# Kernel optimization log

Hardware: AMD Instinct MI355X
Metric: run time of the kernel (lower is better)

Reference implementation:

```python
import jax, jax.numpy as jnp
import numpy as np

T, IN, M, C, OUT = 8192, 1024, 64, 16, 1024  # time, input, trace, context, output


def _ln(x, eps=1e-5):
    mu = jnp.mean(x, axis=-1, keepdims=True)
    var = jnp.var(x, axis=-1, keepdims=True)
    return (x - mu) * jax.lax.rsqrt(var + eps)


def _mish(x):
    return x * jnp.tanh(jax.nn.softplus(x))


def setup_inputs() -> dict:
    key = jax.random.key(0)
    ks = jax.random.split(key, 8)

    def w(k, o, i):
        return (jax.random.normal(k, (o, i), jnp.float32) / np.sqrt(i).astype(np.float32))

    return {
        "x": jax.random.normal(ks[0], (T, IN), jnp.float32),
        "state0": jnp.zeros((1, M, C), jnp.float32),  # real part of complex zero init
        "start": jax.random.uniform(ks[1], (T,)) < 0.002,  # sparse episode resets
        "next_done": jnp.zeros((T,), bool),  # unused by the sequential-equivalent math
        "a": jnp.linspace(1e-6, 0.5, M, dtype=jnp.float32),  # ffa.init decay
        "bf": (2.0 * jnp.pi / jnp.linspace(1.0, 1024.0, C)).astype(jnp.float32),  # ffa.init freqs
        "pre_w": w(ks[2], M, IN), "pre_b": jnp.zeros((M,), jnp.float32),
        "skip_w": w(ks[3], OUT, IN), "skip_b": jnp.zeros((OUT,), jnp.float32),
        "mix_w1": w(ks[4], M * C, 2 * M * C), "mix_b1": jnp.zeros((M * C,), jnp.float32),
        "mix_w2": w(ks[5], M * C, M * C), "mix_b2": jnp.zeros((M * C,), jnp.float32),
        "mix_w3": w(ks[6], OUT, M * C), "mix_b3": jnp.zeros((OUT,), jnp.float32),
    }


def _forward(x, state0, start, a, bf, pre_w, pre_b, skip_w, skip_b,
             mix_w1, mix_b1, mix_w2, mix_b2, mix_w3, mix_b3):
    Tn = x.shape[0]
    # pre = softplus(Linear(LayerNorm(x)))  -> [T, M]
    pre = jax.nn.softplus(_ln(x) @ pre_w.T + pre_b)
    # one-step FFA decay gamma[m,c] = exp(-|a_m| + i*b_c)
    la = jnp.broadcast_to(-jnp.abs(a)[:, None], (a.shape[0], bf.shape[0]))
    lb = jnp.broadcast_to(bf[None, :], la.shape)
    gamma = jnp.exp(jax.lax.complex(la, lb))  # [M, C] complex64
    # reset monoid: s_t = A_t * s_{t-1} + b_t,  A_t = 0 where episode starts
    A = jnp.where(start[:, None, None], jnp.zeros((), gamma.dtype), gamma[None])  # [T,M,C]
    b_el = jnp.broadcast_to(pre[:, :, None].astype(gamma.dtype), A.shape)  # [T,M,C]
    s_init = state0.astype(gamma.dtype)  # [1, M, C]
    b_el = b_el.at[0].add(A[0] * s_init[0])  # fold carried state into first element

    def combine(lhs, rhs):
        Al, bl = lhs
        Ar, br = rhs
        return Ar * Al, Ar * bl + br

    _, s = jax.lax.associative_scan(combine, (A, b_el))  # s: [T, M, C] states at every t

    s_flat = s.reshape(Tn, M * C)
    # global (all-element) complex mean / real std normalization, as in the source
    scaled = (s_flat - jnp.mean(s_flat)) / (1e-6 + jnp.std(s_flat))
    z = jnp.concatenate([scaled.real, scaled.imag], axis=-1)  # [T, 2*M*C]
    z = _mish(z @ mix_w1.T + mix_b1)
    z = _mish(z @ mix_w2.T + mix_b2)
    z = z @ mix_w3.T + mix_b3  # [T, OUT]
    out = _ln(z + (x @ skip_w.T + skip_b))
    return out, s[-1:]


def reference(x, state0, start, next_done, a, bf, pre_w, pre_b, skip_w, skip_b,
              mix_w1, mix_b1, mix_w2, mix_b2, mix_w3, mix_b3):
    return _forward(x, state0, start, a, bf, pre_w, pre_b, skip_w, skip_b,
                    mix_w1, mix_b1, mix_w2, mix_b2, mix_w3, mix_b3)
```

## Files before the change

### kernel.cpp

```cpp
#include <hip/hip_runtime.h>
#include <hip/hip_bf16.h>

#define T_    8192
#define INDIM 1024
#define MTR   64
#define CCTX  16
#define MC    1024
#define NOUT  1024
#define CHUNK 64
#define NCH   128

using bf16x8 = __attribute__((ext_vector_type(8))) short;
using f32x4  = __attribute__((ext_vector_type(4))) float;

__device__ __forceinline__ unsigned short f2bf(float f) {
  unsigned int u = __builtin_bit_cast(unsigned int, f);
  u += 0x7fffu + ((u >> 16) & 1u);
  return (unsigned short)(u >> 16);
}
__device__ __forceinline__ float bf2f(unsigned short u) {
  return __builtin_bit_cast(float, (unsigned int)u << 16);
}

__device__ __forceinline__ float mish_f(float v) {
  float u = __expf(v);
  float w = u * (u + 2.f);
  return (v > 20.f) ? v : v * __fdividef(w, w + 2.f);
}

typedef __attribute__((address_space(1))) void gas_void;
typedef __attribute__((address_space(3))) void las_void;

__device__ __forceinline__ void gload_lds16(const void* g, void* l) {
  __builtin_amdgcn_global_load_lds((gas_void*)g, (las_void*)l, 16, 0, 0);
}

__global__ __launch_bounds__(256) void cast4_k(const float* __restrict__ w1, const float* __restrict__ w2,
                                               const float* __restrict__ w3, const float* __restrict__ sw,
                                               unsigned short* __restrict__ o1, unsigned short* __restrict__ o2,
                                               unsigned short* __restrict__ o3, unsigned short* __restrict__ o4) {
  long i = ((long)blockIdx.x * 256 + threadIdx.x) * 4;
  const float* src; unsigned short* dst; long off;
  if (i < 2097152)      { src = w1; dst = o1; off = i; }
  else if (i < 3145728) { src = w2; dst = o2; off = i - 2097152; }
  else if (i < 4194304) { src = w3; dst = o3; off = i - 3145728; }
  else if (i < 5242880) { src = sw; dst = o4; off = i - 4194304; }
  else return;
  float4 v = *(const float4*)(src + off);
  ushort4 o = { f2bf(v.x), f2bf(v.y), f2bf(v.z), f2bf(v.w) };
  *(ushort4*)(dst + off) = o;
}

__device__ __forceinline__ float2 block_sum2(float s, float ss, float* sbuf) {
#pragma unroll
  for (int off = 32; off > 0; off >>= 1) {
    s  += __shfl_down(s, off);
    ss += __shfl_down(ss, off);
  }
  if ((threadIdx.x & 63) == 0) {
    sbuf[(threadIdx.x >> 6) * 2]     = s;
    sbuf[(threadIdx.x >> 6) * 2 + 1] = ss;
  }
  __syncthreads();
  return make_float2(sbuf[0] + sbuf[2] + sbuf[4] + sbuf[6],
                     sbuf[1] + sbuf[3] + sbuf[5] + sbuf[7]);
}

__global__ __launch_bounds__(256) void wsum_k(const float* __restrict__ w1,
                                              float* __restrict__ wre, float* __restrict__ wim) {
  __shared__ float sbuf[8];
  const long row = blockIdx.x;
  const float4* r4 = (const float4*)(w1 + row * 2048);
  float4 a = r4[threadIdx.x];
  float4 b = r4[256 + threadIdx.x];
  float2 t = block_sum2(a.x + a.y + a.z + a.w, b.x + b.y + b.z + b.w, sbuf);
  if (threadIdx.x == 0) { wre[row] = t.x; wim[row] = t.y; }
}

__global__ __launch_bounds__(256) void ln_cast_k(const float* __restrict__ x,
                                                 float2* __restrict__ rowstat,
                                                 unsigned short* __restrict__ xb) {
  __shared__ float sbuf[8];
  const long row = blockIdx.x;
  float4 v = ((const float4*)(x + (row << 10)))[threadIdx.x];
  ushort4 c = { f2bf(v.x), f2bf(v.y), f2bf(v.z), f2bf(v.w) };
  ((ushort4*)(xb + (row << 10)))[threadIdx.x] = c;
  float2 t = block_sum2(v.x + v.y + v.z + v.w,
                        v.x * v.x + v.y * v.y + v.z * v.z + v.w * v.w, sbuf);
  float mean = t.x * (1.f / 1024.f);
  float var  = t.y * (1.f / 1024.f) - mean * mean;
  float rstd = rsqrtf(var + 1e-5f);
  if (threadIdx.x == 0) rowstat[row] = make_float2(mean, rstd);
}

__global__ __launch_bounds__(256) void ln_out1b_k(const unsigned short* __restrict__ p, float* __restrict__ out) {
  __shared__ float sbuf[8];
  const long row = blockIdx.x;
  ushort4 u4 = ((const ushort4*)(p + (row << 10)))[threadIdx.x];
  float4 v = { bf2f(u4.x), bf2f(u4.y), bf2f(u4.z), bf2f(u4.w) };
  float2 t = block_sum2(v.x + v.y + v.z + v.w,
                        v.x * v.x + v.y * v.y + v.z * v.z + v.w * v.w, sbuf);
  float mean = t.x * (1.f / 1024.f);
  float var  = t.y * (1.f / 1024.f) - mean * mean;
  float rstd = rsqrtf(var + 1e-5f);
  float4 o = { (v.x - mean) * rstd, (v.y - mean) * rstd,
               (v.z - mean) * rstd, (v.w - mean) * rstd };
  ((float4*)(out + (row << 10)))[threadIdx.x] = o;
}

__global__ __launch_bounds__(256) void pre_part_k(const float* __restrict__ x,
                                                  const float2* __restrict__ rowstat,
                                                  const float* __restrict__ pw,
                                                  float* __restrict__ part) {
  const int lane = threadIdx.x & 63;
  const int wvu  = __builtin_amdgcn_readfirstlane(threadIdx.x >> 6);
  const int kc   = blockIdx.y;
  const int r0   = (blockIdx.x * 4 + wvu) * 32;

  const float* wrow = pw + (long)lane * 1024 + kc * 128;
  float wreg[128];
#pragma unroll
  for (int j = 0; j < 32; ++j)
    *(float4*)&wreg[j * 4] = ((const float4*)wrow)[j];
  float swsum = 0.f;
#pragma unroll
  for (int j = 0; j < 128; ++j) swsum += wreg[j];

  float* po = part + ((long)kc * T_ + r0) * 64 + lane;
  const float* xbase = x + (long)r0 * 1024 + kc * 128;

  for (int i = 0; i < 32; i += 2) {
    const float4* xr0 = (const float4*)(xbase + (long)i * 1024);
    const float4* xr1 = (const float4*)(xbase + (long)(i + 1) * 1024);
    float a0 = 0.f, a1 = 0.f, a2 = 0.f, a3 = 0.f;
    float b0 = 0.f, b1 = 0.f, b2 = 0.f, b3 = 0.f;
#pragma unroll
    for (int j = 0; j < 32; j += 4) {
      float4 xa0 = xr0[j],     xa1 = xr0[j + 1], xa2 = xr0[j + 2], xa3 = xr0[j + 3];
      float4 xb0 = xr1[j],     xb1 = xr1[j + 1], xb2 = xr1[j + 2], xb3 = xr1[j + 3];
      a0 += wreg[4*j+0]*xa0.x  + wreg[4*j+1]*xa0.y  + wreg[4*j+2]*xa0.z  + wreg[4*j+3]*xa0.w;
      a1 += wreg[4*j+4]*xa1.x  + wreg[4*j+5]*xa1.y  + wreg[4*j+6]*xa1.z  + wreg[4*j+7]*xa1.w;
      a2 += wreg[4*j+8]*xa2.x  + wreg[4*j+9]*xa2.y  + wreg[4*j+10]*xa2.z + wreg[4*j+11]*xa2.w;
      a3 += wreg[4*j+12]*xa3.x + wreg[4*j+13]*xa3.y + wreg[4*j+14]*xa3.z + wreg[4*j+15]*xa3.w;
      b0 += wreg[4*j+0]*xb0.x  + wreg[4*j+1]*xb0.y  + wreg[4*j+2]*xb0.z  + wreg[4*j+3]*xb0.w;
      b1 += wreg[4*j+4]*xb1.x  + wreg[4*j+5]*xb1.y  + wreg[4*j+6]*xb1.z  + wreg[4*j+7]*xb1.w;
      b2 += wreg[4*j+8]*xb2.x  + wreg[4*j+9]*xb2.y  + wreg[4*j+10]*xb2.z + wreg[4*j+11]*xb2.w;
      b3 += wreg[4*j+12]*xb3.x + wreg[4*j+13]*xb3.y + wreg[4*j+14]*xb3.z + wreg[4*j+15]*xb3.w;
    }
    float2 s0 = rowstat[r0 + i];
    float2 s1 = rowstat[r0 + i + 1];
    po[(long)i * 64]       = s0.y * ((a0 + a1) + (a2 + a3)) - s0.x * s0.y * swsum;
    po[(long)(i + 1) * 64] = s1.y * ((b0 + b1) + (b2 + b3)) - s1.x * s1.y * swsum;
  }
}

__global__ __launch_bounds__(256) void pre_fin_k(const float* __restrict__ part,
                                                 const float* __restrict__ pb,
                                                 float* __restrict__ pre) {
  long i = (long)blockIdx.x * 256 + threadIdx.x;
  int m = (int)(i & 63);
  float s = 0.f;
#pragma unroll
  for (int kc = 0; kc < 8; ++kc)
    s += part[(long)kc * T_ * 64 + i];
  float v = s + pb[m];
  float sp = fmaxf(v, 0.f) + log1pf(expf(-fabsf(v)));
  pre[i] = sp;
}

__global__ __launch_bounds__(256) void scan_p1(const float* __restrict__ pre, const int* __restrict__ start,
                                               const float* __restrict__ a, const float* __restrict__ bfr,
                                               double2* __restrict__ chA, double2* __restrict__ chB) {
  int ch = blockIdx.y * 256 + threadIdx.x;
  int m = ch >> 4, c = ch & 15;
  double dec = exp(-fabs((double)a[m]));
  double th = (double)bfr[c];
  double gre = dec * cos(th), gim = dec * sin(th);
  int j = blockIdx.x;
  int t0 = j * CHUNK;
  double pr = 1.0, pi = 0.0, sr = 0.0, si = 0.0;
  for (int t = t0; t < t0 + CHUNK; ++t) {
    double b = (double)pre[(long)t * 64 + m];
    if (start[t]) {
      pr = 0.0; pi = 0.0; sr = b; si = 0.0;
    } else {
      double nsr = gre * sr - gim * si + b;
      si = gre * si + gim * sr; sr = nsr;
      double npr = gre * pr - gim * pi;
      pi = gre * pi + gim * pr; pr = npr;
    }
  }
  chA[j * MC + ch] = make_double2(pr, pi);
  chB[j * MC + ch] = make_double2(sr, si);
}

__global__ __launch_bounds__(64) void scan_p2(const double2* __restrict__ chA, const double2* __restrict__ chB,
                                              const float* __restrict__ state0,
                                              double2* __restrict__ carry, double* __restrict__ red,
                                              float* __restrict__ out_tail, int fmt) {
  if (blockIdx.x == 0 && threadIdx.x < 4) red[threadIdx.x] = 0.0;
  int ch = blockIdx.x * 64 + threadIdx.x;
  double cr = (double)state0[ch], ci = 0.0;
  for (int j = 0; j < NCH; ++j) {
    carry[j * MC + ch] = make_double2(cr, ci);
    double2 A = chA[j * MC + ch];
    double2 B = chB[j * MC + ch];
    double ncr = A.x * cr - A.y * ci + B.x;
    ci = A.x * ci + A.y * cr + B.y;
    cr = ncr;
  }
  if (fmt == 1024) {
    out_tail[ch] = (float)cr;
  } else {
    out_tail[2 * ch]     = (float)cr;
    out_tail[2 * ch + 1] = (float)ci;
  }
}

__global__ __launch_bounds__(256) void scan_p3(const float* __restrict__ pre, const int* __restrict__ start,
                                               const float* __restrict__ a, const float* __restrict__ bfr,
                                               const double2* __restrict__ carry,
                                               double* __restrict__ red,
                                               unsigned short* __restrict__ z) {
  __shared__ double sbuf[12];
  int ch = blockIdx.y * 256 + threadIdx.x;
  int m = ch >> 4, c = ch & 15;
  double dec = exp(-fabs((double)a[m]));
  double th = (double)bfr[c];
  double gre = dec * cos(th), gim = dec * sin(th);
  int j = blockIdx.x;
  int t0 = j * CHUNK;
  double2 cin = carry[j * MC + ch];
  double sr = cin.x, si = cin.y;
  double aR = 0.0, aI = 0.0, aS = 0.0;
  for (int t = t0; t < t0 + CHUNK; ++t) {
    double b = (double)pre[(long)t * 64 + m];
    if (start[t]) { sr = b; si = 0.0; }
    else {
      double nsr = gre * sr - gim * si + b;
      si = gre * si + gim * sr; sr = nsr;
    }
    z[(long)t * 2048 + ch]        = f2bf((float)sr);
    z[(long)t * 2048 + 1024 + ch] = f2bf((float)si);
    aR += sr; aI += si; aS += sr * sr + si * si;
  }
#pragma unroll
  for (int off = 32; off > 0; off >>= 1) {
    aR += __shfl_down(aR, off); aI += __shfl_down(aI, off); aS += __shfl_down(aS, off);
  }
  if ((threadIdx.x & 63) == 0) {
    int w = threadIdx.x >> 6;
    sbuf[w * 3] = aR; sbuf[w * 3 + 1] = aI; sbuf[w * 3 + 2] = aS;
  }
  __syncthreads();
  if (threadIdx.x == 0) {
    atomicAdd(&red[0], sbuf[0] + sbuf[3] + sbuf[6] + sbuf[9]);
    atomicAdd(&red[1], sbuf[1] + sbuf[4] + sbuf[7] + sbuf[10]);
    atomicAdd(&red[2], sbuf[2] + sbuf[5] + sbuf[8] + sbuf[11]);
  }
}

__global__ void finalize_red(const double* __restrict__ red, float* __restrict__ redf) {
  const double n = (double)T_ * (double)MC;
  double mre = red[0] / n, mim = red[1] / n;
  double var = red[2] / n - mre * mre - mim * mim;
  double sd = sqrt(var > 0.0 ? var : 0.0);
  redf[0] = (float)mre;
  redf[1] = (float)mim;
  redf[2] = (float)(1.0 / (1e-6 + sd));
}

#define TSZ (128 * 32)
template<int EP>
__device__ __forceinline__ void gemm128_core(const unsigned short* __restrict__ A,
                                             const unsigned short* __restrict__ B,
                                             const float* __restrict__ bias,
                                             const unsigned short* __restrict__ addb,
                                             const float* __restrict__ redf,
                                             const float* __restrict__ wre,
                                             const float* __restrict__ wim,
                                             void* __restrict__ Cout,
                                             int bx, int by, int N_, int K_,
                                             unsigned short* lA, unsigned short* lB) {
  const int tid = threadIdx.x;
  const int lane = tid & 63;
  const int wv = tid >> 6;
  const int wr = wv >> 1, wc = wv & 1;
  const long brow = (long)bx * 128;
  const long bcol = (long)by * 128;

  f32x4 acc[4][4];
#pragma unroll
  for (int i = 0; i < 4; i++)
#pragma unroll
    for (int j = 0; j < 4; j++)
      acc[i][j] = f32x4{0.f, 0.f, 0.f, 0.f};

  const int c0 = tid, c1 = tid + 256;
  const long ar0 = brow + (c0 >> 2), ar1 = brow + (c1 >> 2);
  const long br0 = bcol + (c0 >> 2), br1 = bcol + (c1 >> 2);
  const int ko0 = (((c0 & 3) ^ ((c0 >> 3) & 3)) * 8);
  const int ko1 = (((c1 & 3) ^ ((c1 >> 3) & 3)) * 8);
  const int r15 = lane & 15;
  const int swzq = (((lane >> 4) ^ ((r15 >> 1) & 3)) * 8);

  const int nt = K_ >> 5;

#define STAGE(ti, bu)                                                      \
  do {                                                                     \
    gload_lds16(A + ar0 * K_ + (ti) * 32 + ko0, lA + (bu) * TSZ + c0 * 8); \
    gload_lds16(A + ar1 * K_ + (ti) * 32 + ko1, lA + (bu) * TSZ + c1 * 8); \
    gload_lds16(B + br0 * K_ + (ti) * 32 + ko0, lB + (bu) * TSZ + c0 * 8); \
    gload_lds16(B + br1 * K_ + (ti) * 32 + ko1, lB + (bu) * TSZ + c1 * 8); \
  } while (0)

  STAGE(0, 0);
  STAGE(1, 1);

  for (int i = 0; i < nt; ++i) {
    if (i + 2 < nt) {
      STAGE(i + 2, (i + 2) & 3);
      asm volatile("s_waitcnt vmcnt(8)" ::: "memory");
    } else if (i + 1 < nt) {
      asm volatile("s_waitcnt vmcnt(4)" ::: "memory");
    } else {
      asm volatile("s_waitcnt vmcnt(0)" ::: "memory");
    }
    __builtin_amdgcn_sched_barrier(0);
    __builtin_amdgcn_s_barrier();
    __builtin_amdgcn_sched_barrier(0);

    const unsigned short* bA = lA + (i & 3) * TSZ;
    const unsigned short* bB = lB + (i & 3) * TSZ;
    bf16x8 af[4], bv[4];
#pragma unroll
    for (int mi = 0; mi < 4; mi++)
      af[mi] = *(const bf16x8*)&bA[(wr * 64 + mi * 16 + r15) * 32 + swzq];
#pragma unroll
    for (int nj = 0; nj < 4; nj++)
      bv[nj] = *(const bf16x8*)&bB[(wc * 64 + nj * 16 + r15) * 32 + swzq];
#pragma unroll
    for (int mi = 0; mi < 4; mi++)
#pragma unroll
      for (int nj = 0; nj < 4; nj++)
        acc[mi][nj] = __builtin_amdgcn_mfma_f32_16x16x32_bf16(af[mi], bv[nj], acc[mi][nj], 0, 0, 0);
  }
#undef STAGE

  float cre = 0.f, cim = 0.f, inv = 1.f;
  if (EP == 4) { cre = redf[0]; cim = redf[1]; inv = redf[2]; }

  const int rq = (lane >> 4) * 4;
#pragma unroll
  for (int nj = 0; nj < 4; nj++) {
    const long col = bcol + wc * 64 + nj * 16 + r15;
    const float bs = bias[col];
    float wrc = 0.f, wic = 0.f;
    if (EP == 4) { wrc = wre[col]; wic = wim[col]; }
#pragma unroll
    for (int mi = 0; mi < 4; mi++) {
#pragma unroll
      for (int r = 0; r < 4; r++) {
        const long row = brow + wr * 64 + mi * 16 + rq + r;
        float va = acc[mi][nj][r];
        if (EP == 1) {
          ((unsigned short*)Cout)[row * N_ + col] = f2bf(va + bs);
        } else if (EP == 3) {
          float v = va + bs + bf2f(addb[row * N_ + col]);
          ((unsigned short*)Cout)[row * N_ + col] = f2bf(v);
        } else if (EP == 4) {
          float v = (va - cre * wrc - cim * wic) * inv + bs;
          ((unsigned short*)Cout)[row * N_ + col] = f2bf(mish_f(v));
        } else {
          ((unsigned short*)Cout)[row * N_ + col] = f2bf(mish_f(va + bs));
        }
      }
    }
  }
}

template<int EP>
__global__ __launch_bounds__(256) void gemm128_k(const unsigned short* __restrict__ A,
                                                 const unsigned short* __restrict__ B,
                                                 const float* __restrict__ bias,
                                                 const unsigned short* __restrict__ addb,
                                                 void* __restrict__ Cout, int N_, int K_) {
  __shared__ __align__(16) unsigned short lA[4 * TSZ];
  __shared__ __align__(16) unsigned short lB[4 * TSZ];
  gemm128_core<EP>(A, B, bias, addb, nullptr, nullptr, nullptr, Cout,
                   blockIdx.x, blockIdx.y, N_, K_, lA, lB);
}

__global__ __launch_bounds__(256) void gemm_dual128(const unsigned short* __restrict__ A1,
                                                    const unsigned short* __restrict__ B1,
                                                    const float* __restrict__ bias1,
                                                    unsigned short* __restrict__ C1, int K1,
                                                    const float* __restrict__ redf,
                                                    const float* __restrict__ wre,
                                                    const float* __restrict__ wim,
                                                    const unsigned short* __restrict__ A2,
                                                    const unsigned short* __restrict__ B2,
                                                    const float* __restrict__ bias2,
                                                    unsigned short* __restrict__ C2, int K2) {
  __shared__ __align__(16) unsigned short lA[4 * TSZ];
  __shared__ __align__(16) unsigned short lB[4 * TSZ];
  int b = blockIdx.x;
  if (b < 512) {
    gemm128_core<4>(A1, B1, bias1, nullptr, redf, wre, wim, C1, b & 63, b >> 6, 1024, K1, lA, lB);
  } else {
    b -= 512;
    gemm128_core<1>(A2, B2, bias2, nullptr, nullptr, nullptr, nullptr, C2, b & 63, b >> 6, 1024, K2, lA, lB);
  }
}

extern "C" void kernel_launch(void* const* d_in, const int* in_sizes, int n_in,
                              void* d_out, int out_size, void* d_ws, size_t ws_size,
                              hipStream_t stream) {
  (void)in_sizes; (void)n_in; (void)ws_size;
  const float* x      = (const float*)d_in[0];
  const float* state0 = (const float*)d_in[1];
  const int*   start  = (const int*)d_in[2];
  const float* a      = (const float*)d_in[4];
  const float* bfr    = (const float*)d_in[5];
  const float* pre_w  = (const float*)d_in[6];
  const float* pre_b  = (const float*)d_in[7];
  const float* skip_w = (const float*)d_in[8];
  const float* skip_b = (const float*)d_in[9];
  const float* w1     = (const float*)d_in[10];
  const float* b1     = (const float*)d_in[11];
  const float* w2     = (const float*)d_in[12];
  const float* b2     = (const float*)d_in[13];
  const float* w3     = (const float*)d_in[14];
  const float* b3     = (const float*)d_in[15];

  char* ws = (char*)d_ws;
  const size_t MB = 1u << 20;
  unsigned short* skipb = (unsigned short*)(ws + 0);
  float*          part  = (float*)(ws + 32 * MB);
  unsigned short* h3b   = (unsigned short*)(ws + 48 * MB);
  unsigned short* z     = (unsigned short*)(ws + 64 * MB);
  unsigned short* xb    = (unsigned short*)(ws + 96 * MB);
  unsigned short* h2    = (unsigned short*)(ws + 96 * MB);
  unsigned short* h1    = (unsigned short*)(ws + 112 * MB);
  unsigned short* wb1   = (unsigned short*)(ws + 128 * MB);
  unsigned short* wb2   = (unsigned short*)(ws + 132 * MB);
  unsigned short* wb3   = (unsigned short*)(ws + 134 * MB);
  unsigned short* skwb  = (unsigned short*)(ws + 136 * MB);
  float*          pre   = (float*)(ws + 138 * MB);
  double2*        chA   = (double2*)(ws + 140 * MB);
  double2*        chB   = (double2*)(ws + 142 * MB);
  double2*        carry = (double2*)(ws + 144 * MB);
  double*         red   = (double*)(ws + 146 * MB);
  float*          redf  = (float*)(ws + 146 * MB + 64);
  float2*         rowst = (float2*)(ws + 147 * MB);
  float*          wre   = (float*)(ws + 147 * MB + 65536);
  float*          wim   = (float*)(ws + 147 * MB + 65536 + 4096);

  cast4_k<<<5120, 256, 0, stream>>>(w1, w2, w3, skip_w, wb1, wb2, wb3, skwb);
  wsum_k<<<1024, 256, 0, stream>>>(w1, wre, wim);

  ln_cast_k<<<8192, 256, 0, stream>>>(x, rowst, xb);
  pre_part_k<<<dim3(64, 8), 256, 0, stream>>>(x, rowst, pre_w, part);
  pre_fin_k<<<2048, 256, 0, stream>>>(part, pre_b, pre);

  int tail_elems = out_size - T_ * NOUT;
  float* out_tail = (float*)d_out + (long)T_ * NOUT;
  scan_p1<<<dim3(NCH, 4), 256, 0, stream>>>(pre, start, a, bfr, chA, chB);
  scan_p2<<<16, 64, 0, stream>>>(chA, chB, state0, carry, red, out_tail, tail_elems);
  scan_p3<<<dim3(NCH, 4), 256, 0, stream>>>(pre, start, a, bfr, carry, red, z);
  finalize_red<<<1, 1, 0, stream>>>(red, redf);

  gemm_dual128<<<1024, 256, 0, stream>>>(z, wb1, b1, h1, 2048, redf, wre, wim,
                                         xb, skwb, skip_b, skipb, 1024);
  gemm128_k<2><<<dim3(64, 8), 256, 0, stream>>>(h1, wb2, b2, nullptr, h2, 1024, 1024);
  gemm128_k<3><<<dim3(64, 8), 256, 0, stream>>>(h2, wb3, b3, skipb, h3b, 1024, 1024);

  ln_out1b_k<<<8192, 256, 0, stream>>>(h3b, (float*)d_out);
}
```

Baseline: 277.9 us.

## Merge prep kernels, fuse pre projection, add MFMA priority and XCD-aware block remap

Folds the weight-cast, weight row-sum and LayerNorm-stat kernels into one launch. It replaces the split-K pre projection plus its reduction kernel with a single kernel that loops over all K chunks and applies softplus directly, so the partial-sum buffer goes away. It also raises wave priority around the MFMA block in the GEMM core and remaps block indices so that blocks landing on the same XCD work on neighbouring tiles, aiming for better L2 reuse. These changes cut launch overhead and intermediate traffic, but the pre projection now runs only 256 blocks with a serial K loop, which lowers its parallelism.

```diff
diff --git a/kernel.cpp b/kernel.cpp
--- a/kernel.cpp
+++ b/kernel.cpp
@@ -35,22 +35,6 @@
   __builtin_amdgcn_global_load_lds((gas_void*)g, (las_void*)l, 16, 0, 0);
 }
 
-__global__ __launch_bounds__(256) void cast4_k(const float* __restrict__ w1, const float* __restrict__ w2,
-                                               const float* __restrict__ w3, const float* __restrict__ sw,
-                                               unsigned short* __restrict__ o1, unsigned short* __restrict__ o2,
-                                               unsigned short* __restrict__ o3, unsigned short* __restrict__ o4) {
-  long i = ((long)blockIdx.x * 256 + threadIdx.x) * 4;
-  const float* src; unsigned short* dst; long off;
-  if (i < 2097152)      { src = w1; dst = o1; off = i; }
-  else if (i < 3145728) { src = w2; dst = o2; off = i - 2097152; }
-  else if (i < 4194304) { src = w3; dst = o3; off = i - 3145728; }
-  else if (i < 5242880) { src = sw; dst = o4; off = i - 4194304; }
-  else return;
-  float4 v = *(const float4*)(src + off);
-  ushort4 o = { f2bf(v.x), f2bf(v.y), f2bf(v.z), f2bf(v.w) };
-  *(ushort4*)(dst + off) = o;
-}
-
 __device__ __forceinline__ float2 block_sum2(float s, float ss, float* sbuf) {
 #pragma unroll
   for (int off = 32; off > 0; off >>= 1) {
@@ -66,31 +50,45 @@
                      sbuf[1] + sbuf[3] + sbuf[5] + sbuf[7]);
 }
 
-__global__ __launch_bounds__(256) void wsum_k(const float* __restrict__ w1,
-                                              float* __restrict__ wre, float* __restrict__ wim) {
+__global__ __launch_bounds__(256) void prep_k(const float* __restrict__ w1, const float* __restrict__ w2,
+                                              const float* __restrict__ w3, const float* __restrict__ sw,
+                                              const float* __restrict__ x,
+                                              unsigned short* __restrict__ o1, unsigned short* __restrict__ o2,
+                                              unsigned short* __restrict__ o3, unsigned short* __restrict__ o4,
+                                              float* __restrict__ wre, float* __restrict__ wim,
+                                              float2* __restrict__ rowstat, unsigned short* __restrict__ xb) {
   __shared__ float sbuf[8];
-  const long row = blockIdx.x;
-  const float4* r4 = (const float4*)(w1 + row * 2048);
-  float4 a = r4[threadIdx.x];
-  float4 b = r4[256 + threadIdx.x];
-  float2 t = block_sum2(a.x + a.y + a.z + a.w, b.x + b.y + b.z + b.w, sbuf);
-  if (threadIdx.x == 0) { wre[row] = t.x; wim[row] = t.y; }
-}
-
-__global__ __launch_bounds__(256) void ln_cast_k(const float* __restrict__ x,
-                                                 float2* __restrict__ rowstat,
-                                                 unsigned short* __restrict__ xb) {
-  __shared__ float sbuf[8];
-  const long row = blockIdx.x;
-  float4 v = ((const float4*)(x + (row << 10)))[threadIdx.x];
-  ushort4 c = { f2bf(v.x), f2bf(v.y), f2bf(v.z), f2bf(v.w) };
-  ((ushort4*)(xb + (row << 10)))[threadIdx.x] = c;
-  float2 t = block_sum2(v.x + v.y + v.z + v.w,
-                        v.x * v.x + v.y * v.y + v.z * v.z + v.w * v.w, sbuf);
-  float mean = t.x * (1.f / 1024.f);
-  float var  = t.y * (1.f / 1024.f) - mean * mean;
-  float rstd = rsqrtf(var + 1e-5f);
-  if (threadIdx.x == 0) rowstat[row] = make_float2(mean, rstd);
+  const int b = blockIdx.x;
+  if (b < 5120) {
+    long i = ((long)b * 256 + threadIdx.x) * 4;
+    const float* src; unsigned short* dst; long off;
+    if (i < 2097152)      { src = w1; dst = o1; off = i; }
+    else if (i < 3145728) { src = w2; dst = o2; off = i - 2097152; }
+    else if (i < 4194304) { src = w3; dst = o3; off = i - 3145728; }
+    else if (i < 5242880) { src = sw; dst = o4; off = i - 4194304; }
+    else return;
+    float4 v = *(const float4*)(src + off);
+    ushort4 o = { f2bf(v.x), f2bf(v.y), f2bf(v.z), f2bf(v.w) };
+    *(ushort4*)(dst + off) = o;
+  } else if (b < 6144) {
+    const long row = b - 5120;
+    const float4* r4 = (const float4*)(w1 + row * 2048);
+    float4 a = r4[threadIdx.x];
+    float4 c = r4[256 + threadIdx.x];
+    float2 t = block_sum2(a.x + a.y + a.z + a.w, c.x + c.y + c.z + c.w, sbuf);
+    if (threadIdx.x == 0) { wre[row] = t.x; wim[row] = t.y; }
+  } else {
+    const long row = b - 6144;
+    float4 v = ((const float4*)(x + (row << 10)))[threadIdx.x];
+    ushort4 c = { f2bf(v.x), f2bf(v.y), f2bf(v.z), f2bf(v.w) };
+    ((ushort4*)(xb + (row << 10)))[threadIdx.x] = c;
+    float2 t = block_sum2(v.x + v.y + v.z + v.w,
+                          v.x * v.x + v.y * v.y + v.z * v.z + v.w * v.w, sbuf);
+    float mean = t.x * (1.f / 1024.f);
+    float var  = t.y * (1.f / 1024.f) - mean * mean;
+    float rstd = rsqrtf(var + 1e-5f);
+    if (threadIdx.x == 0) rowstat[row] = make_float2(mean, rstd);
+  }
 }
 
 __global__ __launch_bounds__(256) void ln_out1b_k(const unsigned short* __restrict__ p, float* __restrict__ out) {
@@ -108,64 +106,54 @@
   ((float4*)(out + (row << 10)))[threadIdx.x] = o;
 }
 
-__global__ __launch_bounds__(256) void pre_part_k(const float* __restrict__ x,
-                                                  const float2* __restrict__ rowstat,
-                                                  const float* __restrict__ pw,
-                                                  float* __restrict__ part) {
+__global__ __launch_bounds__(256) void pre_lnproj_k(const float* __restrict__ x,
+                                                    const float2* __restrict__ rowstat,
+                                                    const float* __restrict__ pw,
+                                                    const float* __restrict__ pb,
+                                                    float* __restrict__ pre) {
   const int lane = threadIdx.x & 63;
   const int wvu  = __builtin_amdgcn_readfirstlane(threadIdx.x >> 6);
-  const int kc   = blockIdx.y;
-  const int r0   = (blockIdx.x * 4 + wvu) * 32;
-
-  const float* wrow = pw + (long)lane * 1024 + kc * 128;
-  float wreg[128];
-#pragma unroll
-  for (int j = 0; j < 32; ++j)
-    *(float4*)&wreg[j * 4] = ((const float4*)wrow)[j];
+  const int r0   = blockIdx.x * 32 + wvu * 8;
+
+  float acc[8];
+#pragma unroll
+  for (int r = 0; r < 8; ++r) acc[r] = 0.f;
   float swsum = 0.f;
-#pragma unroll
-  for (int j = 0; j < 128; ++j) swsum += wreg[j];
-
-  float* po = part + ((long)kc * T_ + r0) * 64 + lane;
-  const float* xbase = x + (long)r0 * 1024 + kc * 128;
-
-  for (int i = 0; i < 32; i += 2) {
-    const float4* xr0 = (const float4*)(xbase + (long)i * 1024);
-    const float4* xr1 = (const float4*)(xbase + (long)(i + 1) * 1024);
-    float a0 = 0.f, a1 = 0.f, a2 = 0.f, a3 = 0.f;
-    float b0 = 0.f, b1 = 0.f, b2 = 0.f, b3 = 0.f;
-#pragma unroll
-    for (int j = 0; j < 32; j += 4) {
-      float4 xa0 = xr0[j],     xa1 = xr0[j + 1], xa2 = xr0[j + 2], xa3 = xr0[j + 3];
-      float4 xb0 = xr1[j],     xb1 = xr1[j + 1], xb2 = xr1[j + 2], xb3 = xr1[j + 3];
-      a0 += wreg[4*j+0]*xa0.x  + wreg[4*j+1]*xa0.y  + wreg[4*j+2]*xa0.z  + wreg[4*j+3]*xa0.w;
-      a1 += wreg[4*j+4]*xa1.x  + wreg[4*j+5]*xa1.y  + wreg[4*j+6]*xa1.z  + wreg[4*j+7]*xa1.w;
-      a2 += wreg[4*j+8]*xa2.x  + wreg[4*j+9]*xa2.y  + wreg[4*j+10]*xa2.z + wreg[4*j+11]*xa2.w;
-      a3 += wreg[4*j+12]*xa3.x + wreg[4*j+13]*xa3.y + wreg[4*j+14]*xa3.z + wreg[4*j+15]*xa3.w;
-      b0 += wreg[4*j+0]*xb0.x  + wreg[4*j+1]*xb0.y  + wreg[4*j+2]*xb0.z  + wreg[4*j+3]*xb0.w;
-      b1 += wreg[4*j+4]*xb1.x  + wreg[4*j+5]*xb1.y  + wreg[4*j+6]*xb1.z  + wreg[4*j+7]*xb1.w;
-      b2 += wreg[4*j+8]*xb2.x  + wreg[4*j+9]*xb2.y  + wreg[4*j+10]*xb2.z + wreg[4*j+11]*xb2.w;
-      b3 += wreg[4*j+12]*xb3.x + wreg[4*j+13]*xb3.y + wreg[4*j+14]*xb3.z + wreg[4*j+15]*xb3.w;
+
+  for (int kc = 0; kc < 8; ++kc) {
+    float wreg[128];
+    const float4* wrow4 = (const float4*)(pw + (long)lane * 1024 + kc * 128);
+#pragma unroll
+    for (int j = 0; j < 32; ++j)
+      *(float4*)&wreg[j * 4] = wrow4[j];
+#pragma unroll
+    for (int j = 0; j < 128; ++j) swsum += wreg[j];
+
+    const float* xbase = x + (long)r0 * 1024 + kc * 128;
+#pragma unroll
+    for (int r = 0; r < 8; ++r) {
+      const float4* xr = (const float4*)(xbase + (long)r * 1024);
+      float s0 = 0.f, s1 = 0.f, s2 = 0.f, s3 = 0.f;
+#pragma unroll
+      for (int j = 0; j < 32; j += 4) {
+        float4 x0 = xr[j], x1 = xr[j + 1], x2 = xr[j + 2], x3 = xr[j + 3];
+        s0 += wreg[4*j+0]*x0.x  + wreg[4*j+1]*x0.y  + wreg[4*j+2]*x0.z  + wreg[4*j+3]*x0.w;
+        s1 += wreg[4*j+4]*x1.x  + wreg[4*j+5]*x1.y  + wreg[4*j+6]*x1.z  + wreg[4*j+7]*x1.w;
+        s2 += wreg[4*j+8]*x2.x  + wreg[4*j+9]*x2.y  + wreg[4*j+10]*x2.z + wreg[4*j+11]*x2.w;
+        s3 += wreg[4*j+12]*x3.x + wreg[4*j+13]*x3.y + wreg[4*j+14]*x3.z + wreg[4*j+15]*x3.w;
+      }
+      acc[r] += (s0 + s1) + (s2 + s3);
     }
-    float2 s0 = rowstat[r0 + i];
-    float2 s1 = rowstat[r0 + i + 1];
-    po[(long)i * 64]       = s0.y * ((a0 + a1) + (a2 + a3)) - s0.x * s0.y * swsum;
-    po[(long)(i + 1) * 64] = s1.y * ((b0 + b1) + (b2 + b3)) - s1.x * s1.y * swsum;
-  }
-}
-
-__global__ __launch_bounds__(256) void pre_fin_k(const float* __restrict__ part,
-                                                 const float* __restrict__ pb,
-                                                 float* __restrict__ pre) {
-  long i = (long)blockIdx.x * 256 + threadIdx.x;
-  int m = (int)(i & 63);
-  float s = 0.f;
-#pragma unroll
-  for (int kc = 0; kc < 8; ++kc)
-    s += part[(long)kc * T_ * 64 + i];
-  float v = s + pb[m];
-  float sp = fmaxf(v, 0.f) + log1pf(expf(-fabsf(v)));
-  pre[i] = sp;
+  }
+
+  const float bias = pb[lane];
+#pragma unroll
+  for (int r = 0; r < 8; ++r) {
+    float2 st = rowstat[r0 + r];
+    float v = st.y * acc[r] - st.x * st.y * swsum + bias;
+    float sp = fmaxf(v, 0.f) + log1pf(expf(-fabsf(v)));
+    pre[(long)(r0 + r) * 64 + lane] = sp;
+  }
 }
 
 __global__ __launch_bounds__(256) void scan_p1(const float* __restrict__ pre, const int* __restrict__ start,
@@ -339,11 +327,13 @@
 #pragma unroll
     for (int nj = 0; nj < 4; nj++)
       bv[nj] = *(const bf16x8*)&bB[(wc * 64 + nj * 16 + r15) * 32 + swzq];
+    __builtin_amdgcn_s_setprio(1);
 #pragma unroll
     for (int mi = 0; mi < 4; mi++)
 #pragma unroll
       for (int nj = 0; nj < 4; nj++)
         acc[mi][nj] = __builtin_amdgcn_mfma_f32_16x16x32_bf16(af[mi], bv[nj], acc[mi][nj], 0, 0, 0);
+    __builtin_amdgcn_s_setprio(0);
   }
 #undef STAGE
 
@@ -380,15 +370,16 @@
 }
 
 template<int EP>
-__global__ __launch_bounds__(256) void gemm128_k(const unsigned short* __restrict__ A,
-                                                 const unsigned short* __restrict__ B,
-                                                 const float* __restrict__ bias,
-                                                 const unsigned short* __restrict__ addb,
-                                                 void* __restrict__ Cout, int N_, int K_) {
+__global__ __launch_bounds__(256) void gemm128s_k(const unsigned short* __restrict__ A,
+                                                  const unsigned short* __restrict__ B,
+                                                  const float* __restrict__ bias,
+                                                  const unsigned short* __restrict__ addb,
+                                                  void* __restrict__ Cout, int N_, int K_) {
   __shared__ __align__(16) unsigned short lA[4 * TSZ];
   __shared__ __align__(16) unsigned short lB[4 * TSZ];
+  int comp = (int)((blockIdx.x & 7) * 64 + (blockIdx.x >> 3));
   gemm128_core<EP>(A, B, bias, addb, nullptr, nullptr, nullptr, Cout,
-                   blockIdx.x, blockIdx.y, N_, K_, lA, lB);
+                   comp & 63, comp >> 6, N_, K_, lA, lB);
 }
 
 __global__ __launch_bounds__(256) void gemm_dual128(const unsigned short* __restrict__ A1,
@@ -404,12 +395,12 @@
                                                     unsigned short* __restrict__ C2, int K2) {
   __shared__ __align__(16) unsigned short lA[4 * TSZ];
   __shared__ __align__(16) unsigned short lB[4 * TSZ];
-  int b = blockIdx.x;
-  if (b < 512) {
-    gemm128_core<4>(A1, B1, bias1, nullptr, redf, wre, wim, C1, b & 63, b >> 6, 1024, K1, lA, lB);
+  int comp = (int)((blockIdx.x & 7) * 128 + (blockIdx.x >> 3));
+  if (comp < 512) {
+    gemm128_core<4>(A1, B1, bias1, nullptr, redf, wre, wim, C1, comp & 63, comp >> 6, 1024, K1, lA, lB);
   } else {
-    b -= 512;
-    gemm128_core<1>(A2, B2, bias2, nullptr, nullptr, nullptr, nullptr, C2, b & 63, b >> 6, 1024, K2, lA, lB);
+    comp -= 512;
+    gemm128_core<1>(A2, B2, bias2, nullptr, nullptr, nullptr, nullptr, C2, comp & 63, comp >> 6, 1024, K2, lA, lB);
   }
 }
 
@@ -436,7 +427,6 @@
   char* ws = (char*)d_ws;
   const size_t MB = 1u << 20;
   unsigned short* skipb = (unsigned short*)(ws + 0);
-  float*          part  = (float*)(ws + 32 * MB);
   unsigned short* h3b   = (unsigned short*)(ws + 48 * MB);
   unsigned short* z     = (unsigned short*)(ws + 64 * MB);
   unsigned short* xb    = (unsigned short*)(ws + 96 * MB);
@@ -456,12 +446,10 @@
   float*          wre   = (float*)(ws + 147 * MB + 65536);
   float*          wim   = (float*)(ws + 147 * MB + 65536 + 4096);
 
-  cast4_k<<<5120, 256, 0, stream>>>(w1, w2, w3, skip_w, wb1, wb2, wb3, skwb);
-  wsum_k<<<1024, 256, 0, stream>>>(w1, wre, wim);
-
-  ln_cast_k<<<8192, 256, 0, stream>>>(x, rowst, xb);
-  pre_part_k<<<dim3(64, 8), 256, 0, stream>>>(x, rowst, pre_w, part);
-  pre_fin_k<<<2048, 256, 0, stream>>>(part, pre_b, pre);
+  prep_k<<<14336, 256, 0, stream>>>(w1, w2, w3, skip_w, x,
+                                    wb1, wb2, wb3, skwb, wre, wim, rowst, xb);
+
+  pre_lnproj_k<<<256, 256, 0, stream>>>(x, rowst, pre_w, pre_b, pre);
 
   int tail_elems = out_size - T_ * NOUT;
   float* out_tail = (float*)d_out + (long)T_ * NOUT;
@@ -472,8 +460,8 @@
 
   gemm_dual128<<<1024, 256, 0, stream>>>(z, wb1, b1, h1, 2048, redf, wre, wim,
                                          xb, skwb, skip_b, skipb, 1024);
-  gemm128_k<2><<<dim3(64, 8), 256, 0, stream>>>(h1, wb2, b2, nullptr, h2, 1024, 1024);
-  gemm128_k<3><<<dim3(64, 8), 256, 0, stream>>>(h2, wb3, b3, skipb, h3b, 1024, 1024);
+  gemm128s_k<2><<<512, 256, 0, stream>>>(h1, wb2, b2, nullptr, h2, 1024, 1024);
+  gemm128s_k<3><<<512, 256, 0, stream>>>(h2, wb3, b3, skipb, h3b, 1024, 1024);
 
   ln_out1b_k<<<8192, 256, 0, stream>>>(h3b, (float*)d_out);
 }
```

New measurement: 398.5 us. 43.4% more time.

## Fuse prep kernels, swizzle GEMM block order for XCDs, raise MFMA priority

Applied to the files above, without the earlier changes.

Merges the weight cast, W1 row-sum and x layernorm-stat/cast kernels into one launch, removing two kernel launches. Remaps GEMM block indices so consecutive blocks, which are dispatched round-robin across the 8 XCDs, land on tiles that share operands, for better L2 reuse. Wraps the MFMA loop in s_setprio to favour math waves. Also moves the partial-sum workspace offset.

```diff
diff --git a/kernel.cpp b/kernel.cpp
--- a/kernel.cpp
+++ b/kernel.cpp
@@ -35,22 +35,6 @@
   __builtin_amdgcn_global_load_lds((gas_void*)g, (las_void*)l, 16, 0, 0);
 }
 
-__global__ __launch_bounds__(256) void cast4_k(const float* __restrict__ w1, const float* __restrict__ w2,
-                                               const float* __restrict__ w3, const float* __restrict__ sw,
-                                               unsigned short* __restrict__ o1, unsigned short* __restrict__ o2,
-                                               unsigned short* __restrict__ o3, unsigned short* __restrict__ o4) {
-  long i = ((long)blockIdx.x * 256 + threadIdx.x) * 4;
-  const float* src; unsigned short* dst; long off;
-  if (i < 2097152)      { src = w1; dst = o1; off = i; }
-  else if (i < 3145728) { src = w2; dst = o2; off = i - 2097152; }
-  else if (i < 4194304) { src = w3; dst = o3; off = i - 3145728; }
-  else if (i < 5242880) { src = sw; dst = o4; off = i - 4194304; }
-  else return;
-  float4 v = *(const float4*)(src + off);
-  ushort4 o = { f2bf(v.x), f2bf(v.y), f2bf(v.z), f2bf(v.w) };
-  *(ushort4*)(dst + off) = o;
-}
-
 __device__ __forceinline__ float2 block_sum2(float s, float ss, float* sbuf) {
 #pragma unroll
   for (int off = 32; off > 0; off >>= 1) {
@@ -66,31 +50,45 @@
                      sbuf[1] + sbuf[3] + sbuf[5] + sbuf[7]);
 }
 
-__global__ __launch_bounds__(256) void wsum_k(const float* __restrict__ w1,
-                                              float* __restrict__ wre, float* __restrict__ wim) {
+__global__ __launch_bounds__(256) void prep_k(const float* __restrict__ w1, const float* __restrict__ w2,
+                                              const float* __restrict__ w3, const float* __restrict__ sw,
+                                              const float* __restrict__ x,
+                                              unsigned short* __restrict__ o1, unsigned short* __restrict__ o2,
+                                              unsigned short* __restrict__ o3, unsigned short* __restrict__ o4,
+                                              float* __restrict__ wre, float* __restrict__ wim,
+                                              float2* __restrict__ rowstat, unsigned short* __restrict__ xb) {
   __shared__ float sbuf[8];
-  const long row = blockIdx.x;
-  const float4* r4 = (const float4*)(w1 + row * 2048);
-  float4 a = r4[threadIdx.x];
-  float4 b = r4[256 + threadIdx.x];
-  float2 t = block_sum2(a.x + a.y + a.z + a.w, b.x + b.y + b.z + b.w, sbuf);
-  if (threadIdx.x == 0) { wre[row] = t.x; wim[row] = t.y; }
-}
-
-__global__ __launch_bounds__(256) void ln_cast_k(const float* __restrict__ x,
-                                                 float2* __restrict__ rowstat,
-                                                 unsigned short* __restrict__ xb) {
-  __shared__ float sbuf[8];
-  const long row = blockIdx.x;
-  float4 v = ((const float4*)(x + (row << 10)))[threadIdx.x];
-  ushort4 c = { f2bf(v.x), f2bf(v.y), f2bf(v.z), f2bf(v.w) };
-  ((ushort4*)(xb + (row << 10)))[threadIdx.x] = c;
-  float2 t = block_sum2(v.x + v.y + v.z + v.w,
-                        v.x * v.x + v.y * v.y + v.z * v.z + v.w * v.w, sbuf);
-  float mean = t.x * (1.f / 1024.f);
-  float var  = t.y * (1.f / 1024.f) - mean * mean;
-  float rstd = rsqrtf(var + 1e-5f);
-  if (threadIdx.x == 0) rowstat[row] = make_float2(mean, rstd);
+  const int b = blockIdx.x;
+  if (b < 5120) {
+    long i = ((long)b * 256 + threadIdx.x) * 4;
+    const float* src; unsigned short* dst; long off;
+    if (i < 2097152)      { src = w1; dst = o1; off = i; }
+    else if (i < 3145728) { src = w2; dst = o2; off = i - 2097152; }
+    else if (i < 4194304) { src = w3; dst = o3; off = i - 3145728; }
+    else if (i < 5242880) { src = sw; dst = o4; off = i - 4194304; }
+    else return;
+    float4 v = *(const float4*)(src + off);
+    ushort4 o = { f2bf(v.x), f2bf(v.y), f2bf(v.z), f2bf(v.w) };
+    *(ushort4*)(dst + off) = o;
+  } else if (b < 6144) {
+    const long row = b - 5120;
+    const float4* r4 = (const float4*)(w1 + row * 2048);
+    float4 a = r4[threadIdx.x];
+    float4 c = r4[256 + threadIdx.x];
+    float2 t = block_sum2(a.x + a.y + a.z + a.w, c.x + c.y + c.z + c.w, sbuf);
+    if (threadIdx.x == 0) { wre[row] = t.x; wim[row] = t.y; }
+  } else {
+    const long row = b - 6144;
+    float4 v = ((const float4*)(x + (row << 10)))[threadIdx.x];
+    ushort4 c = { f2bf(v.x), f2bf(v.y), f2bf(v.z), f2bf(v.w) };
+    ((ushort4*)(xb + (row << 10)))[threadIdx.x] = c;
+    float2 t = block_sum2(v.x + v.y + v.z + v.w,
+                          v.x * v.x + v.y * v.y + v.z * v.z + v.w * v.w, sbuf);
+    float mean = t.x * (1.f / 1024.f);
+    float var  = t.y * (1.f / 1024.f) - mean * mean;
+    float rstd = rsqrtf(var + 1e-5f);
+    if (threadIdx.x == 0) rowstat[row] = make_float2(mean, rstd);
+  }
 }
 
 __global__ __launch_bounds__(256) void ln_out1b_k(const unsigned short* __restrict__ p, float* __restrict__ out) {
@@ -339,11 +337,13 @@
 #pragma unroll
     for (int nj = 0; nj < 4; nj++)
       bv[nj] = *(const bf16x8*)&bB[(wc * 64 + nj * 16 + r15) * 32 + swzq];
+    __builtin_amdgcn_s_setprio(1);
 #pragma unroll
     for (int mi = 0; mi < 4; mi++)
 #pragma unroll
       for (int nj = 0; nj < 4; nj++)
         acc[mi][nj] = __builtin_amdgcn_mfma_f32_16x16x32_bf16(af[mi], bv[nj], acc[mi][nj], 0, 0, 0);
+    __builtin_amdgcn_s_setprio(0);
   }
 #undef STAGE
 
@@ -380,15 +380,16 @@
 }
 
 template<int EP>
-__global__ __launch_bounds__(256) void gemm128_k(const unsigned short* __restrict__ A,
-                                                 const unsigned short* __restrict__ B,
-                                                 const float* __restrict__ bias,
-                                                 const unsigned short* __restrict__ addb,
-                                                 void* __restrict__ Cout, int N_, int K_) {
+__global__ __launch_bounds__(256) void gemm128s_k(const unsigned short* __restrict__ A,
+                                                  const unsigned short* __restrict__ B,
+                                                  const float* __restrict__ bias,
+                                                  const unsigned short* __restrict__ addb,
+                                                  void* __restrict__ Cout, int N_, int K_) {
   __shared__ __align__(16) unsigned short lA[4 * TSZ];
   __shared__ __align__(16) unsigned short lB[4 * TSZ];
+  int comp = (int)((blockIdx.x & 7) * 64 + (blockIdx.x >> 3));
   gemm128_core<EP>(A, B, bias, addb, nullptr, nullptr, nullptr, Cout,
-                   blockIdx.x, blockIdx.y, N_, K_, lA, lB);
+                   comp & 63, comp >> 6, N_, K_, lA, lB);
 }
 
 __global__ __launch_bounds__(256) void gemm_dual128(const unsigned short* __restrict__ A1,
@@ -404,12 +405,12 @@
                                                     unsigned short* __restrict__ C2, int K2) {
   __shared__ __align__(16) unsigned short lA[4 * TSZ];
   __shared__ __align__(16) unsigned short lB[4 * TSZ];
-  int b = blockIdx.x;
-  if (b < 512) {
-    gemm128_core<4>(A1, B1, bias1, nullptr, redf, wre, wim, C1, b & 63, b >> 6, 1024, K1, lA, lB);
+  int comp = (int)((blockIdx.x & 7) * 128 + (blockIdx.x >> 3));
+  if (comp < 512) {
+    gemm128_core<4>(A1, B1, bias1, nullptr, redf, wre, wim, C1, comp & 63, comp >> 6, 1024, K1, lA, lB);
   } else {
-    b -= 512;
-    gemm128_core<1>(A2, B2, bias2, nullptr, nullptr, nullptr, nullptr, C2, b & 63, b >> 6, 1024, K2, lA, lB);
+    comp -= 512;
+    gemm128_core<1>(A2, B2, bias2, nullptr, nullptr, nullptr, nullptr, C2, comp & 63, comp >> 6, 1024, K2, lA, lB);
   }
 }
 
@@ -436,7 +437,7 @@
   char* ws = (char*)d_ws;
   const size_t MB = 1u << 20;
   unsigned short* skipb = (unsigned short*)(ws + 0);
-  float*          part  = (float*)(ws + 32 * MB);
+  float*          part  = (float*)(ws + 16 * MB);
   unsigned short* h3b   = (unsigned short*)(ws + 48 * MB);
   unsigned short* z     = (unsigned short*)(ws + 64 * MB);
   unsigned short* xb    = (unsigned short*)(ws + 96 * MB);
@@ -456,10 +457,9 @@
   float*          wre   = (float*)(ws + 147 * MB + 65536);
   float*          wim   = (float*)(ws + 147 * MB + 65536 + 4096);
 
-  cast4_k<<<5120, 256, 0, stream>>>(w1, w2, w3, skip_w, wb1, wb2, wb3, skwb);
-  wsum_k<<<1024, 256, 0, stream>>>(w1, wre, wim);
-
-  ln_cast_k<<<8192, 256, 0, stream>>>(x, rowst, xb);
+  prep_k<<<14336, 256, 0, stream>>>(w1, w2, w3, skip_w, x,
+                                    wb1, wb2, wb3, skwb, wre, wim, rowst, xb);
+
   pre_part_k<<<dim3(64, 8), 256, 0, stream>>>(x, rowst, pre_w, part);
   pre_fin_k<<<2048, 256, 0, stream>>>(part, pre_b, pre);
 
@@ -472,8 +472,8 @@
 
   gemm_dual128<<<1024, 256, 0, stream>>>(z, wb1, b1, h1, 2048, redf, wre, wim,
                                          xb, skwb, skip_b, skipb, 1024);
-  gemm128_k<2><<<dim3(64, 8), 256, 0, stream>>>(h1, wb2, b2, nullptr, h2, 1024, 1024);
-  gemm128_k<3><<<dim3(64, 8), 256, 0, stream>>>(h2, wb3, b3, skipb, h3b, 1024, 1024);
+  gemm128s_k<2><<<512, 256, 0, stream>>>(h1, wb2, b2, nullptr, h2, 1024, 1024);
+  gemm128s_k<3><<<512, 256, 0, stream>>>(h2, wb3, b3, skipb, h3b, 1024, 1024);
 
   ln_out1b_k<<<8192, 256, 0, stream>>>(h3b, (float*)d_out);
 }
```

Result: slower. 319.0 us (+14.8%).
